# Performance work log

Hardware: AMD Instinct MI355X
Metric: run time of the kernel (lower is better)

## Reference

```python
import jax, jax.numpy as jnp
import numpy as np

SEQ_LEN, BATCH, TAGS = 512, 128, 48
START_TAG, END_TAG = 46, 47  # y_map['<s>'], y_map['<eof>']


def setup_inputs() -> dict:
    key = jax.random.key(0)
    k1, k2 = jax.random.split(key)
    scores = jax.random.normal(k1, (SEQ_LEN, BATCH, TAGS, TAGS), dtype=jnp.float32)
    target = jax.random.randint(k2, (SEQ_LEN, BATCH), 0, TAGS * TAGS, dtype=jnp.int64)
    mask = jnp.ones((SEQ_LEN, BATCH), dtype=bool)
    return {"scores": scores, "target": target, "mask": mask}


def reference(scores, target, mask):
    S, B, T, _ = scores.shape
    # gold path energy: gather from flattened (from_tag, to_tag) dim, masked sum
    flat = scores.reshape(S, B, T * T)
    tg = jnp.take_along_axis(flat, target[:, :, None], axis=2)[..., 0]  # (S, B)
    tg_energy = jnp.sum(jnp.where(mask, tg, jnp.zeros((), scores.dtype)))
    # forward algorithm (log-sum-exp recurrence over seq)
    part0 = scores[0, :, START_TAG, :]  # (B, T)
    def step(partition, xm):
        cur_values, m = xm  # (B, T, T), (B,)
        cur_partition = jax.nn.logsumexp(cur_values + partition[:, :, None], axis=1)  # (B, T)
        partition = jnp.where(m[:, None], cur_partition, partition)
        return partition, None
    partition, _ = jax.lax.scan(step, part0, (scores[1:], mask[1:]))
    log_Z = jnp.sum(partition[:, END_TAG])
    return (log_Z - tg_energy) / B
```

## Files before the change

### kernel.cpp

```cpp
#include <hip/hip_runtime.h>


#define S_LEN 512
#define BATCH 128
#define T 48
#define TT 2304
#define START_TAG 46
#define END_TAG 47

#define CHUNK 32
#define NCHUNK 16
#define NTASK (NCHUNK * BATCH)
#define P1_WAVES 4
#define P1_THREADS 256
#define P1_BLOCKS (NTASK / P1_WAVES)
#define SIGMA 0.0078125f

typedef float f32x4 __attribute__((ext_vector_type(4)));
typedef short bf16x8 __attribute__((ext_vector_type(8)));
typedef short bf16x4 __attribute__((ext_vector_type(4)));

__device__ __forceinline__ short f2bf(float x) {
  unsigned u = __float_as_uint(x);
  u = (u + 0x7fffu + ((u >> 16) & 1u)) >> 16;
  return (short)u;
}

#if __has_builtin(__builtin_amdgcn_exp2f)
#define EXPS(x) __builtin_amdgcn_exp2f(fmaf((x), 1.44269504089f, -7.0f))
#define EXP1(x) __builtin_amdgcn_exp2f((x) * 1.44269504089f)
#else
#define EXPS(x) (__expf(x) * SIGMA)
#define EXP1(x) __expf(x)
#endif

#if __has_builtin(__builtin_amdgcn_mfma_f32_16x16x16bf16_1k)
#define MFMA16(a, b, c) __builtin_amdgcn_mfma_f32_16x16x16bf16_1k((a), (b), (c), 0, 0, 0)
#else
static __device__ __forceinline__ f32x4 mfma16_asm(bf16x4 a, bf16x4 b, f32x4 c) {
  f32x4 d;
  asm volatile("v_mfma_f32_16x16x16_bf16 %0, %1, %2, %3\n\ts_nop 7"
               : "=v"(d) : "v"(a), "v"(b), "v"(c));
  return d;
}
#define MFMA16(a, b, c) mfma16_asm((a), (b), (c))
#endif

struct Raw { float r24[24]; float r12[12]; };

#define CRF_LOAD(RW, PE) do {                                                  \
  const float* q0_ = (PE) + (size_t)(8 * g) * T + c15;                         \
  _Pragma("unroll") for (int ti = 0; ti < 3; ++ti)                             \
    _Pragma("unroll") for (int i = 0; i < 8; ++i)                              \
      (RW).r24[ti * 8 + i] = q0_[(size_t)i * T + 16 * ti];                     \
  const float* q1_ = (PE) + (size_t)(32 + 4 * g) * T + c15;                    \
  _Pragma("unroll") for (int ti = 0; ti < 3; ++ti)                             \
    _Pragma("unroll") for (int i = 0; i < 4; ++i)                              \
      (RW).r12[ti * 4 + i] = q1_[(size_t)i * T + 16 * ti];                     \
} while (0)

#define CRF_STEP(RW, KK, RECYC) do {                                           \
  const int msk_ = __shfl(mt, (KK), 64);                                       \
  const bool id_ = (msk_ == 0);                                                \
  bf16x8 A32_[3]; bf16x4 A16_[3];                                              \
  _Pragma("unroll") for (int ti = 0; ti < 3; ++ti) {                           \
    bf16x8 av_;                                                                \
    _Pragma("unroll") for (int i = 0; i < 8; ++i) {                            \
      float v_ = id_ ? (((8 * g + i) == (16 * ti + c15)) ? SIGMA : 0.f)        \
                     : EXPS((RW).r24[ti * 8 + i]);                             \
      av_[i] = f2bf(v_);                                                       \
    }                                                                          \
    A32_[ti] = av_;                                                            \
    bf16x4 aw_;                                                                \
    _Pragma("unroll") for (int i = 0; i < 4; ++i) {                            \
      float v_ = id_ ? (((32 + 4 * g + i) == (16 * ti + c15)) ? SIGMA : 0.f)   \
                     : EXPS((RW).r12[ti * 4 + i]);                             \
      aw_[i] = f2bf(v_);                                                       \
    }                                                                          \
    A16_[ti] = aw_;                                                            \
  }                                                                            \
  _Pragma("unroll") for (int ti = 0; ti < 3; ++ti)                             \
    _Pragma("unroll") for (int tj = 0; tj < 3; ++tj)                           \
      Cf[ti][tj] = __builtin_amdgcn_mfma_f32_16x16x32_bf16(A32_[ti], Bf32[tj], zz, 0, 0, 0); \
  _Pragma("unroll") for (int ti = 0; ti < 3; ++ti)                             \
    _Pragma("unroll") for (int tj = 0; tj < 3; ++tj)                           \
      Cf[ti][tj] = MFMA16(A16_[ti], Bf16[tj], Cf[ti][tj]);                     \
  if (RECYC) {                                                                 \
    _Pragma("unroll") for (int tj = 0; tj < 3; ++tj) {                         \
      bf16x8 b0_; bf16x4 b1_;                                                  \
      const int sLo_ = ((g & 1) << 5) + c15;                                   \
      _Pragma("unroll") for (int i = 0; i < 8; ++i) {                          \
        const int r_ = i & 3;                                                  \
        const int s_ = sLo_ + ((i & 4) ? 16 : 0);                              \
        float a0_ = __shfl(Cf[0][tj][r_], s_, 64);                             \
        float a1_ = __shfl(Cf[1][tj][r_], s_, 64);                             \
        b0_[i] = f2bf((g >> 1) ? a1_ : a0_);                                   \
      }                                                                        \
      _Pragma("unroll") for (int i = 0; i < 4; ++i) b1_[i] = f2bf(Cf[2][tj][i]); \
      Bf32[tj] = b0_; Bf16[tj] = b1_;                                          \
    }                                                                          \
  }                                                                            \
} while (0)

__global__ __launch_bounds__(P1_THREADS, 2) void crf_chunk(
    const float* __restrict__ scores, const int* __restrict__ target,
    const int* __restrict__ mask, float* __restrict__ Rbuf,
    float* __restrict__ tgbuf)
{
  const int t = threadIdx.x;
  const int lane = t & 63;
  const int wid = t >> 6;
  const int g = lane >> 4;
  const int c15 = lane & 15;

  const int task = blockIdx.x * P1_WAVES + wid;
  const int b = task & (BATCH - 1);
  const int cIdx = task >> 7;
  const int s0 = cIdx * CHUNK;

  int mt;
  {
    int sl = s0 + (lane & 31);
    mt = (lane < 32) ? mask[(size_t)sl * BATCH + b]
                     : target[(size_t)sl * BATCH + b];
  }

  float tg = 0.f;
  {
    int tgt_l = __shfl(mt, 32 + (lane & 31), 64);
    if (lane < CHUNK && mt)
      tg = scores[((size_t)(s0 + lane) * BATCH + b) * TT + tgt_l];
  }

  const float* sb0 = scores + ((size_t)s0 * BATCH + b) * TT;

  Raw rA, rB;
  CRF_LOAD(rA, sb0 + (size_t)BATCH * TT);

  const int msk0 = __shfl(mt, 0, 64);
  const bool id0 = (s0 == 0) || (msk0 == 0);
  bf16x8 Bf32[3];
  bf16x4 Bf16[3];
#pragma unroll
  for (int tj = 0; tj < 3; ++tj) {
    const int col = 16 * tj + c15;
    bf16x8 bv;
#pragma unroll
    for (int i = 0; i < 8; ++i) {
      int kk = 8 * g + i;
      float val = id0 ? ((kk == col) ? 1.f : 0.f)
                      : EXP1(sb0[(size_t)col * T + kk]);
      bv[i] = f2bf(val);
    }
    Bf32[tj] = bv;
    bf16x4 bw;
#pragma unroll
    for (int i = 0; i < 4; ++i) {
      int kk = 32 + 4 * g + i;
      float val = id0 ? ((kk == col) ? 1.f : 0.f)
                      : EXP1(sb0[(size_t)col * T + kk]);
      bw[i] = f2bf(val);
    }
    Bf16[tj] = bw;
  }

  f32x4 Cf[3][3];
  const f32x4 zz = {0.f, 0.f, 0.f, 0.f};

  int k = 1;
#pragma unroll 1
  for (; k + 1 < CHUNK; k += 2) {
    CRF_LOAD(rB, sb0 + (size_t)(k + 1) * BATCH * TT);
    CRF_STEP(rA, k, 1);
    CRF_LOAD(rA, sb0 + (size_t)(k + 2) * BATCH * TT);
    CRF_STEP(rB, k + 1, 1);
  }
  CRF_STEP(rA, k, 0);

  float* outp = Rbuf + (size_t)((size_t)cIdx * BATCH + b) * TT;
#pragma unroll
  for (int ti = 0; ti < 3; ++ti)
#pragma unroll
    for (int tj = 0; tj < 3; ++tj)
#pragma unroll
      for (int r = 0; r < 4; ++r) {
        int j = 16 * ti + 4 * g + r;
        int icol = 16 * tj + c15;
        outp[j * T + icol] = Cf[ti][tj][r];
      }

#pragma unroll
  for (int d = 1; d < 64; d <<= 1) tg += __shfl_xor(tg, d, 64);
  if (lane == 0) tgbuf[task] = tg;
}

__global__ __launch_bounds__(64) void crf_fold(
    const float* __restrict__ scores, const float* __restrict__ Rbuf,
    float* __restrict__ pend)
{
  __shared__ __align__(16) float e[T];
  const int b = blockIdx.x;
  const int j = threadIdx.x & 63;
  const int jr = (j < T) ? j : (T - 1);
  float p = (j < T) ? scores[(size_t)b * TT + START_TAG * T + j] : -1e30f;

  float4 bufA[12], bufB[12];
  {
    const float4* rA = (const float4*)(Rbuf + ((size_t)0 * BATCH + b) * TT + (size_t)jr * T);
#pragma unroll
    for (int q = 0; q < 12; ++q) bufA[q] = rA[q];
  }

#pragma unroll 1
  for (int c = 0; c < NCHUNK; c += 2) {
    const float4* rB = (const float4*)(Rbuf + ((size_t)(c + 1) * BATCH + b) * TT + (size_t)jr * T);
#pragma unroll
    for (int q = 0; q < 12; ++q) bufB[q] = rB[q];

    {
      float sh = __shfl(p, 0, 64);
      float ev = __expf(p - sh);
      if (j < T) e[j] = ev;
      asm volatile("s_waitcnt lgkmcnt(0)" ::: "memory");
      float acc = 0.f;
#pragma unroll
      for (int q = 0; q < 12; ++q) {
        float4 ef = ((const float4*)e)[q];
        acc += ef.x * bufA[q].x; acc += ef.y * bufA[q].y;
        acc += ef.z * bufA[q].z; acc += ef.w * bufA[q].w;
      }
      p = sh + __logf(acc);
    }
    if (c + 2 < NCHUNK) {
      const float4* rA = (const float4*)(Rbuf + ((size_t)(c + 2) * BATCH + b) * TT + (size_t)jr * T);
#pragma unroll
      for (int q = 0; q < 12; ++q) bufA[q] = rA[q];
    }
    {
      float sh = __shfl(p, 0, 64);
      float ev = __expf(p - sh);
      if (j < T) e[j] = ev;
      asm volatile("s_waitcnt lgkmcnt(0)" ::: "memory");
      float acc = 0.f;
#pragma unroll
      for (int q = 0; q < 12; ++q) {
        float4 ef = ((const float4*)e)[q];
        acc += ef.x * bufB[q].x; acc += ef.y * bufB[q].y;
        acc += ef.z * bufB[q].z; acc += ef.w * bufB[q].w;
      }
      p = sh + __logf(acc);
    }
  }
  if (j == END_TAG) pend[b] = p;
}

__global__ void crf_final(const float* __restrict__ pend, const float* __restrict__ tgbuf,
                          float* __restrict__ out)
{
  __shared__ float sp[256], st2[256];
  int t = threadIdx.x;
  float ps = (t < BATCH) ? pend[t] : 0.f;
  float ts = 0.f;
  for (int q = t; q < NTASK; q += 256) ts += tgbuf[q];
  sp[t] = ps; st2[t] = ts;
  __syncthreads();
  for (int off = 128; off > 0; off >>= 1) {
    if (t < off) { sp[t] += sp[t + off]; st2[t] += st2[t + off]; }
    __syncthreads();
  }
  if (t == 0) {
    const float corr = 496.0f * 4.852030263919617f;
    out[0] = (sp[0] - st2[0]) / (float)BATCH + corr;
  }
}

__global__ __launch_bounds__(512) void fb_scan(
    const float* __restrict__ scores, const int* __restrict__ target,
    const int* __restrict__ mask, float* __restrict__ ws)
{
  __shared__ float tile[2][TT];
  __shared__ float p[T];
  __shared__ float red_m[8][T];
  __shared__ float red_s[8][T];
  __shared__ int lmask[S_LEN];
  __shared__ int ltgt[S_LEN];

  const int b = blockIdx.x;
  const int t = threadIdx.x;
  const int j = t & 63;
  const int ic = t >> 6;
  const bool valid = (j < T);

  lmask[t] = mask[(size_t)t * BATCH + b];
  ltgt[t] = target[(size_t)t * BATCH + b];
  {
    const float4* src = (const float4*)(scores + (size_t)b * TT);
    float4 r0 = src[t]; float4 r1;
    if (t < 64) r1 = src[512 + t];
    float4* dst = (float4*)tile[0];
    dst[t] = r0;
    if (t < 64) dst[512 + t] = r1;
  }
  __syncthreads();
  float tg_local = 0.0f;
  for (int s = 0; s < S_LEN; ++s) {
    const int buf = s & 1;
    float4 r0, r1;
    if (s + 1 < S_LEN) {
      const float4* src = (const float4*)(scores + ((size_t)(s + 1) * BATCH + b) * TT);
      r0 = src[t];
      if (t < 64) r1 = src[512 + t];
    }
    if (s == 0) {
      if (t < T) p[t] = tile[0][START_TAG * T + t];
      if (t == 0 && lmask[0]) tg_local += tile[0][ltgt[0]];
    } else {
      if (valid) {
        const int i0 = ic * 6;
        float x[6]; float m = -1e30f;
#pragma unroll
        for (int kq = 0; kq < 6; ++kq) {
          x[kq] = tile[buf][(i0 + kq) * T + j] + p[i0 + kq];
          m = fmaxf(m, x[kq]);
        }
        float sum = 0.0f;
#pragma unroll
        for (int kq = 0; kq < 6; ++kq) sum += __expf(x[kq] - m);
        red_m[ic][j] = m; red_s[ic][j] = sum;
      }
      if (t == 0 && lmask[s]) tg_local += tile[buf][ltgt[s]];
    }
    __syncthreads();
    if (s > 0 && t < T) {
      float M = red_m[0][t];
#pragma unroll
      for (int g2 = 1; g2 < 8; ++g2) M = fmaxf(M, red_m[g2][t]);
      float Ssum = 0.0f;
#pragma unroll
      for (int g2 = 0; g2 < 8; ++g2) Ssum += red_s[g2][t] * __expf(red_m[g2][t] - M);
      float cur = M + __logf(Ssum);
      if (lmask[s]) p[t] = cur;
    }
    if (s + 1 < S_LEN) {
      float4* dst = (float4*)tile[buf ^ 1];
      dst[t] = r0;
      if (t < 64) dst[512 + t] = r1;
    }
    __syncthreads();
  }
  if (t == 0) ws[b] = p[END_TAG] - tg_local;
}

__global__ void fb_reduce(const float* __restrict__ ws, float* __restrict__ out)
{
  __shared__ float sh[BATCH];
  const int t = threadIdx.x;
  if (t < BATCH) sh[t] = ws[t];
  __syncthreads();
  if (t == 0) {
    float s = 0.0f;
    for (int k = 0; k < BATCH; ++k) s += sh[k];
    out[0] = s / (float)BATCH;
  }
}

extern "C" void kernel_launch(void* const* d_in, const int* in_sizes, int n_in,
                              void* d_out, int out_size, void* d_ws, size_t ws_size,
                              hipStream_t stream)
{
  const float* scores = (const float*)d_in[0];
  const int* target = (const int*)d_in[1];
  const int* mask = (const int*)d_in[2];
  float* out = (float*)d_out;

  const size_t RB_FLOATS = (size_t)NTASK * TT;
  const size_t need = RB_FLOATS * 4 + (size_t)NTASK * 4 + (size_t)BATCH * 4;

  if (ws_size >= need) {
    float* Rbuf = (float*)d_ws;
    float* tgbuf = Rbuf + RB_FLOATS;
    float* pend = tgbuf + NTASK;
    crf_chunk<<<P1_BLOCKS, P1_THREADS, 0, stream>>>(scores, target, mask, Rbuf, tgbuf);
    crf_fold<<<BATCH, 64, 0, stream>>>(scores, Rbuf, pend);
    crf_final<<<1, 256, 0, stream>>>(pend, tgbuf, out);
  } else {
    float* ws = (float*)d_ws;
    fb_scan<<<BATCH, 512, 0, stream>>>(scores, target, mask, ws);
    fb_reduce<<<1, 128, 0, stream>>>(ws, out);
  }
}
```

Before: 130.7 us.

## Store chunk transfer matrices in bf16 and start chunks from identity

The intermediate per-chunk transfer matrices written by crf_chunk and read by crf_fold are now stored as bf16 instead of fp32, halving that workspace traffic. The initial B operand becomes a constant identity, with the first step folded into the regular MFMA loop, which drops the separate exp-based preload. The fold kernel unpacks bf16 pairs and adds block barriers around the shared exp vector, and the final correction constant is changed to match the new scaling. This loses precision in the stored matrices and adds __syncthreads in the latency-bound sequential fold.

New measurement: 121.5 us. 7.1% less time.

```diff
diff --git a/kernel.cpp b/kernel.cpp
--- a/kernel.cpp
+++ b/kernel.cpp
@@ -28,10 +28,8 @@
 
 #if __has_builtin(__builtin_amdgcn_exp2f)
 #define EXPS(x) __builtin_amdgcn_exp2f(fmaf((x), 1.44269504089f, -7.0f))
-#define EXP1(x) __builtin_amdgcn_exp2f((x) * 1.44269504089f)
 #else
 #define EXPS(x) (__expf(x) * SIGMA)
-#define EXP1(x) __expf(x)
 #endif
 
 #if __has_builtin(__builtin_amdgcn_mfma_f32_16x16x16bf16_1k)
@@ -61,7 +59,7 @@
 
 #define CRF_STEP(RW, KK, RECYC) do {                                           \
   const int msk_ = __shfl(mt, (KK), 64);                                       \
-  const bool id_ = (msk_ == 0);                                                \
+  const bool id_ = (msk_ == 0) || ((s0 == 0) && ((KK) == 0));                  \
   bf16x8 A32_[3]; bf16x4 A16_[3];                                              \
   _Pragma("unroll") for (int ti = 0; ti < 3; ++ti) {                           \
     bf16x8 av_;                                                                \
@@ -104,7 +102,7 @@
 
 __global__ __launch_bounds__(P1_THREADS, 2) void crf_chunk(
     const float* __restrict__ scores, const int* __restrict__ target,
-    const int* __restrict__ mask, float* __restrict__ Rbuf,
+    const int* __restrict__ mask, unsigned short* __restrict__ Rbuf,
     float* __restrict__ tgbuf)
 {
   const int t = threadIdx.x;
@@ -133,12 +131,11 @@
   }
 
   const float* sb0 = scores + ((size_t)s0 * BATCH + b) * TT;
+  const size_t mstride = (size_t)BATCH * TT;
 
   Raw rA, rB;
-  CRF_LOAD(rA, sb0 + (size_t)BATCH * TT);
-
-  const int msk0 = __shfl(mt, 0, 64);
-  const bool id0 = (s0 == 0) || (msk0 == 0);
+  CRF_LOAD(rA, sb0);
+
   bf16x8 Bf32[3];
   bf16x4 Bf16[3];
 #pragma unroll
@@ -146,38 +143,30 @@
     const int col = 16 * tj + c15;
     bf16x8 bv;
 #pragma unroll
-    for (int i = 0; i < 8; ++i) {
-      int kk = 8 * g + i;
-      float val = id0 ? ((kk == col) ? 1.f : 0.f)
-                      : EXP1(sb0[(size_t)col * T + kk]);
-      bv[i] = f2bf(val);
-    }
+    for (int i = 0; i < 8; ++i) bv[i] = ((8 * g + i) == col) ? (short)0x3F80 : (short)0;
     Bf32[tj] = bv;
     bf16x4 bw;
 #pragma unroll
-    for (int i = 0; i < 4; ++i) {
-      int kk = 32 + 4 * g + i;
-      float val = id0 ? ((kk == col) ? 1.f : 0.f)
-                      : EXP1(sb0[(size_t)col * T + kk]);
-      bw[i] = f2bf(val);
-    }
+    for (int i = 0; i < 4; ++i) bw[i] = ((32 + 4 * g + i) == col) ? (short)0x3F80 : (short)0;
     Bf16[tj] = bw;
   }
 
   f32x4 Cf[3][3];
   const f32x4 zz = {0.f, 0.f, 0.f, 0.f};
 
-  int k = 1;
+  int k = 0;
 #pragma unroll 1
-  for (; k + 1 < CHUNK; k += 2) {
-    CRF_LOAD(rB, sb0 + (size_t)(k + 1) * BATCH * TT);
+  for (; k + 2 < CHUNK; k += 2) {
+    CRF_LOAD(rB, sb0 + (size_t)(k + 1) * mstride);
     CRF_STEP(rA, k, 1);
-    CRF_LOAD(rA, sb0 + (size_t)(k + 2) * BATCH * TT);
+    CRF_LOAD(rA, sb0 + (size_t)(k + 2) * mstride);
     CRF_STEP(rB, k + 1, 1);
   }
-  CRF_STEP(rA, k, 0);
-
-  float* outp = Rbuf + (size_t)((size_t)cIdx * BATCH + b) * TT;
+  CRF_LOAD(rB, sb0 + (size_t)31 * mstride);
+  CRF_STEP(rA, 30, 1);
+  CRF_STEP(rB, 31, 0);
+
+  unsigned short* outp = Rbuf + (size_t)((size_t)cIdx * BATCH + b) * TT;
 #pragma unroll
   for (int ti = 0; ti < 3; ++ti)
 #pragma unroll
@@ -186,7 +175,7 @@
       for (int r = 0; r < 4; ++r) {
         int j = 16 * ti + 4 * g + r;
         int icol = 16 * tj + c15;
-        outp[j * T + icol] = Cf[ti][tj][r];
+        outp[j * T + icol] = (unsigned short)f2bf(Cf[ti][tj][r]);
       }
 
 #pragma unroll
@@ -195,7 +184,7 @@
 }
 
 __global__ __launch_bounds__(64) void crf_fold(
-    const float* __restrict__ scores, const float* __restrict__ Rbuf,
+    const float* __restrict__ scores, const unsigned short* __restrict__ Rbuf,
     float* __restrict__ pend)
 {
   __shared__ __align__(16) float e[T];
@@ -204,53 +193,47 @@
   const int jr = (j < T) ? j : (T - 1);
   float p = (j < T) ? scores[(size_t)b * TT + START_TAG * T + j] : -1e30f;
 
-  float4 bufA[12], bufB[12];
+  uint4 bufA[6], bufB[6];
   {
-    const float4* rA = (const float4*)(Rbuf + ((size_t)0 * BATCH + b) * TT + (size_t)jr * T);
-#pragma unroll
-    for (int q = 0; q < 12; ++q) bufA[q] = rA[q];
-  }
+    const uint4* rA = (const uint4*)(Rbuf + ((size_t)0 * BATCH + b) * TT + (size_t)jr * T);
+#pragma unroll
+    for (int q = 0; q < 6; ++q) bufA[q] = rA[q];
+  }
+
+#define FOLD_STEP(BUF) do {                                                    \
+    float sh = __shfl(p, 0, 64);                                               \
+    float ev = __expf(p - sh);                                                 \
+    if (j < T) e[j] = ev;                                                      \
+    asm volatile("s_waitcnt lgkmcnt(0)" ::: "memory");                         \
+    __syncthreads();                                                           \
+    float acc = 0.f;                                                           \
+    _Pragma("unroll") for (int q = 0; q < 6; ++q) {                            \
+      const unsigned* u = (const unsigned*)&(BUF)[q];                          \
+      _Pragma("unroll") for (int h = 0; h < 4; ++h) {                          \
+        float lo = __uint_as_float(u[h] << 16);                                \
+        float hi = __uint_as_float(u[h] & 0xffff0000u);                        \
+        acc += e[q * 8 + 2 * h] * lo;                                          \
+        acc += e[q * 8 + 2 * h + 1] * hi;                                      \
+      }                                                                        \
+    }                                                                          \
+    p = sh + __logf(acc);                                                      \
+    __syncthreads();                                                           \
+  } while (0)
 
 #pragma unroll 1
   for (int c = 0; c < NCHUNK; c += 2) {
-    const float4* rB = (const float4*)(Rbuf + ((size_t)(c + 1) * BATCH + b) * TT + (size_t)jr * T);
-#pragma unroll
-    for (int q = 0; q < 12; ++q) bufB[q] = rB[q];
-
-    {
-      float sh = __shfl(p, 0, 64);
-      float ev = __expf(p - sh);
-      if (j < T) e[j] = ev;
-      asm volatile("s_waitcnt lgkmcnt(0)" ::: "memory");
-      float acc = 0.f;
-#pragma unroll
-      for (int q = 0; q < 12; ++q) {
-        float4 ef = ((const float4*)e)[q];
-        acc += ef.x * bufA[q].x; acc += ef.y * bufA[q].y;
-        acc += ef.z * bufA[q].z; acc += ef.w * bufA[q].w;
-      }
-      p = sh + __logf(acc);
-    }
+    const uint4* rB = (const uint4*)(Rbuf + ((size_t)(c + 1) * BATCH + b) * TT + (size_t)jr * T);
+#pragma unroll
+    for (int q = 0; q < 6; ++q) bufB[q] = rB[q];
+    FOLD_STEP(bufA);
     if (c + 2 < NCHUNK) {
-      const float4* rA = (const float4*)(Rbuf + ((size_t)(c + 2) * BATCH + b) * TT + (size_t)jr * T);
-#pragma unroll
-      for (int q = 0; q < 12; ++q) bufA[q] = rA[q];
-    }
-    {
-      float sh = __shfl(p, 0, 64);
-      float ev = __expf(p - sh);
-      if (j < T) e[j] = ev;
-      asm volatile("s_waitcnt lgkmcnt(0)" ::: "memory");
-      float acc = 0.f;
-#pragma unroll
-      for (int q = 0; q < 12; ++q) {
-        float4 ef = ((const float4*)e)[q];
-        acc += ef.x * bufB[q].x; acc += ef.y * bufB[q].y;
-        acc += ef.z * bufB[q].z; acc += ef.w * bufB[q].w;
-      }
-      p = sh + __logf(acc);
-    }
-  }
+      const uint4* rA = (const uint4*)(Rbuf + ((size_t)(c + 2) * BATCH + b) * TT + (size_t)jr * T);
+#pragma unroll
+      for (int q = 0; q < 6; ++q) bufA[q] = rA[q];
+    }
+    FOLD_STEP(bufB);
+  }
+#undef FOLD_STEP
   if (j == END_TAG) pend[b] = p;
 }
 
@@ -269,7 +252,7 @@
     __syncthreads();
   }
   if (t == 0) {
-    const float corr = 496.0f * 4.852030263919617f;
+    const float corr = 3584.0f * 0.6931471805599453f;
     out[0] = (sp[0] - st2[0]) / (float)BATCH + corr;
   }
 }
@@ -373,12 +356,12 @@
   const int* mask = (const int*)d_in[2];
   float* out = (float*)d_out;
 
-  const size_t RB_FLOATS = (size_t)NTASK * TT;
-  const size_t need = RB_FLOATS * 4 + (size_t)NTASK * 4 + (size_t)BATCH * 4;
+  const size_t RB_BYTES = (size_t)NTASK * TT * 2;
+  const size_t need = RB_BYTES + (size_t)NTASK * 4 + (size_t)BATCH * 4;
 
   if (ws_size >= need) {
-    float* Rbuf = (float*)d_ws;
-    float* tgbuf = Rbuf + RB_FLOATS;
+    unsigned short* Rbuf = (unsigned short*)d_ws;
+    float* tgbuf = (float*)((char*)d_ws + RB_BYTES);
     float* pend = tgbuf + NTASK;
     crf_chunk<<<P1_BLOCKS, P1_THREADS, 0, stream>>>(scores, target, mask, Rbuf, tgbuf);
     crf_fold<<<BATCH, 64, 0, stream>>>(scores, Rbuf, pend);
```
